# Kernel tuning notes

Measured on AMD Instinct MI355X. Metric: run time of the kernel, lower is better.

The kernel has to match this reference:

```python
import jax, jax.numpy as jnp
import numpy as np

OMODE, PMODE, NZ = 2, 4, 8
NY = NX = 512
NPY = NPX = 128
NPOS = 1024
BATCH = 64


def setup_inputs() -> dict:
    key = jax.random.key(0)
    ks = jax.random.split(key, 8)
    obja = jax.random.uniform(ks[0], (OMODE, NZ, NY, NX), jnp.float32, 0.9, 1.0)
    objp = 0.1 * jax.random.normal(ks[1], (OMODE, NZ, NY, NX), jnp.float32)
    probe = jax.random.normal(ks[2], (PMODE, NPY, NPX, 2), jnp.float32)
    probe_pos_shifts = 0.5 * jax.random.normal(ks[3], (NPOS, 2), jnp.float32)
    theta = jax.random.normal(ks[4], (NPY, NPX), jnp.float32)
    H = jnp.stack([jnp.cos(theta), jnp.sin(theta)], axis=-1)  # unit-modulus Fresnel phasor (re, im)
    omode_occu = jax.nn.softmax(jax.random.normal(ks[5], (OMODE,), jnp.float32))
    indices = jax.random.randint(ks[6], (BATCH,), 0, NPOS, jnp.int32)
    crop_pos = jax.random.randint(ks[7], (NPOS, 2), 0, NY - NPY, jnp.int32)
    return {"obja": obja, "objp": objp, "probe": probe,
            "probe_pos_shifts": probe_pos_shifts, "H": H, "omode_occu": omode_occu,
            "indices": indices, "crop_pos": crop_pos}


def reference(obja, objp, probe, probe_pos_shifts, H, omode_occu, indices, crop_pos):
    npy, npx = probe.shape[1], probe.shape[2]
    probe_c = probe[..., 0] + 1j * probe[..., 1]   # (pmode, Npy, Npx) complex64
    H_c = H[..., 0] + 1j * H[..., 1]               # (Npy, Npx) complex64

    # --- indexed patch gather: (omode, nz, N, Npy, Npx) -> (N, omode, nz, Npy, Npx) ---
    cy = crop_pos[indices, 0]
    cx = crop_pos[indices, 1]
    gy = cy[:, None, None] + jnp.arange(npy, dtype=jnp.int32)[None, :, None]  # (N, Npy, 1)
    gx = cx[:, None, None] + jnp.arange(npx, dtype=jnp.int32)[None, None, :]  # (N, 1, Npx)
    pa = jnp.transpose(obja[:, :, gy, gx], (2, 0, 1, 3, 4))
    pp = jnp.transpose(objp[:, :, gy, gx], (2, 0, 1, 3, 4))
    T = pa * jnp.exp(1j * pp)  # transmission per slice, (N, omode, nz, Npy, Npx)

    # --- sub-pixel Fourier probe shifts (imshift_batch) ---
    kpy = jnp.fft.fftfreq(npy).astype(jnp.float32)
    kpx = jnp.fft.fftfreq(npx).astype(jnp.float32)
    sh = probe_pos_shifts[indices]  # (N, 2)
    ramp = jnp.exp(-2j * jnp.pi * (kpy[None, :, None] * sh[:, 0, None, None]
                                   + kpx[None, None, :] * sh[:, 1, None, None]))  # (N, Npy, Npx)
    probes = jnp.fft.ifft2(jnp.fft.fft2(probe_c)[None] * ramp[:, None])  # (N, pmode, Npy, Npx)

    # --- multislice propagation: psi (N, omode, pmode, Npy, Npx) ---
    psi = probes[:, None]
    nz = T.shape[2]
    for z in range(nz):
        psi = psi * T[:, :, z, None]
        if z < nz - 1:
            psi = jnp.fft.ifft2(jnp.fft.fft2(psi) * H_c)

    # --- far-field detector intensity, mode-incoherent sum ---
    dp = jnp.einsum('o,nopyx->nyx', omode_occu, jnp.abs(jnp.fft.fft2(psi)) ** 2)
    return dp
```

## Files before the change

kernel.cpp:

```cpp
#include <hip/hip_runtime.h>

static constexpr int OMODE = 2, PMODE = 4, NZ = 8;
static constexpr int NYX = 512;
static constexpr int NP  = 128;
static constexpr int BATCH = 64;
static constexpr int LSTR = 129;
static constexpr float INV_N2 = 1.0f / 16384.0f;

typedef float v2f __attribute__((ext_vector_type(2)));

__device__ __forceinline__ int br7(int x) { return (int)(__brev((unsigned)x) >> 25); }

__device__ __forceinline__ v2f splat2(float s) { return (v2f){s, s}; }
__device__ __forceinline__ v2f swapv(v2f v) { return __builtin_shufflevector(v, v, 1, 0); }
__device__ __forceinline__ v2f cmulv(v2f a, float br_, float bi_) {
  return a * splat2(br_) + swapv(a) * (v2f){-bi_, bi_};
}
__device__ __forceinline__ v2f cmulvv(v2f a, v2f b) {
  return a * splat2(b.x) + swapv(a) * (v2f){-b.y, b.y};
}

template<int CTRL>
__device__ __forceinline__ float dppf(float x) {
  int i = __float_as_int(x);
  int r = __builtin_amdgcn_update_dpp(i, i, CTRL, 0xF, 0xF, false);
  return __int_as_float(r);
}

struct Tw {
  float tc6, ts6;
  float g[6];
  float dwr[6], dwi[6];
};

template<int CTRL, int S>
__device__ __forceinline__ v2f bfly_dpp(v2f m, const Tw& tw) {
  v2f t = (v2f){dppf<CTRL>(m.x), dppf<CTRL>(m.y)};
  return t + splat2(tw.g[S]) * m;
}
template<int OFS, int S>
__device__ __forceinline__ v2f bfly_swz(v2f m, const Tw& tw) {
  v2f t;
  t.x = __int_as_float(__builtin_amdgcn_ds_swizzle(__float_as_int(m.x), OFS));
  t.y = __int_as_float(__builtin_amdgcn_ds_swizzle(__float_as_int(m.y), OFS));
  return t + splat2(tw.g[S]) * m;
}
__device__ __forceinline__ v2f bfly_bp32(v2f m, int bp32, float g5) {
  v2f t;
  t.x = __int_as_float(__builtin_amdgcn_ds_bpermute(bp32, __float_as_int(m.x)));
  t.y = __int_as_float(__builtin_amdgcn_ds_bpermute(bp32, __float_as_int(m.y)));
  return t + splat2(g5) * m;
}

template<int S> __device__ __forceinline__ v2f twd(v2f d, const Tw& tw) {
  return d * splat2(tw.dwr[S]) + swapv(d) * (v2f){-tw.dwi[S], tw.dwi[S]};
}
template<int S> __device__ __forceinline__ v2f twc(v2f a, const Tw& tw) {
  return a * splat2(tw.dwr[S]) + swapv(a) * (v2f){tw.dwi[S], -tw.dwi[S]};
}

__device__ __forceinline__ void dif128(v2f& A, v2f& B, const Tw& tw, int bp32) {
  {
    v2f d = A - B;
    A = A + B;
    B = d * splat2(tw.tc6) + swapv(d) * (v2f){tw.ts6, -tw.ts6};
  }
  A = twd<5>(bfly_bp32(A, bp32, tw.g[5]), tw);  B = twd<5>(bfly_bp32(B, bp32, tw.g[5]), tw);
  A = twd<4>(bfly_swz<0x401F, 4>(A, tw), tw);   B = twd<4>(bfly_swz<0x401F, 4>(B, tw), tw);
  A = twd<3>(bfly_swz<0x201F, 3>(A, tw), tw);   B = twd<3>(bfly_swz<0x201F, 3>(B, tw), tw);
  A = twd<2>(bfly_swz<0x101F, 2>(A, tw), tw);   B = twd<2>(bfly_swz<0x101F, 2>(B, tw), tw);
  A = twd<1>(bfly_dpp<0x4E, 1>(A, tw), tw);     B = twd<1>(bfly_dpp<0x4E, 1>(B, tw), tw);
  A = bfly_dpp<0xB1, 0>(A, tw);                 B = bfly_dpp<0xB1, 0>(B, tw);
}

__device__ __forceinline__ void dit128(v2f& A, v2f& B, const Tw& tw, int bp32) {
  A = bfly_dpp<0xB1, 0>(A, tw);                 B = bfly_dpp<0xB1, 0>(B, tw);
  A = bfly_dpp<0x4E, 1>(twc<1>(A, tw), tw);     B = bfly_dpp<0x4E, 1>(twc<1>(B, tw), tw);
  A = bfly_swz<0x101F, 2>(twc<2>(A, tw), tw);   B = bfly_swz<0x101F, 2>(twc<2>(B, tw), tw);
  A = bfly_swz<0x201F, 3>(twc<3>(A, tw), tw);   B = bfly_swz<0x201F, 3>(twc<3>(B, tw), tw);
  A = bfly_swz<0x401F, 4>(twc<4>(A, tw), tw);   B = bfly_swz<0x401F, 4>(twc<4>(B, tw), tw);
  A = bfly_bp32(twc<5>(A, tw), bp32, tw.g[5]);  B = bfly_bp32(twc<5>(B, tw), bp32, tw.g[5]);
  {
    v2f m = B * splat2(tw.tc6) + swapv(B) * (v2f){-tw.ts6, tw.ts6};
    B = A - m;
    A = A + m;
  }
}

__device__ __forceinline__ void init_tw(Tw& tw, int lane) {
  tw.g[0] = (lane & 1) ? -1.f : 1.f;
#pragma unroll
  for (int s = 1; s < 6; ++s) {
    int h = 1 << s;
    int j = lane & (h - 1);
    float ang = 3.14159265358979f * (float)j / (float)h;
    float ts_, tc_;
    __sincosf(ang, &ts_, &tc_);
    bool up = (lane >> s) & 1;
    tw.g[s]   = up ? -1.f : 1.f;
    tw.dwr[s] = up ? tc_ : 1.f;
    tw.dwi[s] = up ? -ts_ : 0.f;
  }
  __sincosf(3.14159265358979f * (float)lane * (1.f / 64.f), &tw.ts6, &tw.tc6);
}

__global__ void __launch_bounds__(256) init_hpre(const float* __restrict__ H,
                                                 float2* __restrict__ hp) {
  int i = blockIdx.x * blockDim.x + threadIdx.x;
  if (i >= NP * NP) return;
  int px = i >> 7, py = i & (NP - 1);
  int ky = br7(py), kx = br7(px);
  hp[px * NP + py] = make_float2(H[(ky * NP + kx) * 2 + 0] * INV_N2,
                                 H[(ky * NP + kx) * 2 + 1] * INV_N2);
}

__global__ void __launch_bounds__(256) init_ramp(const float* __restrict__ shifts,
                                                 const int* __restrict__ indices,
                                                 float2* __restrict__ rampy,
                                                 float2* __restrict__ rampx) {
  int i = blockIdx.x * blockDim.x + threadIdx.x;
  if (i >= 2 * BATCH * NP) return;
  int which = (i >= BATCH * NP) ? 1 : 0;
  int r = i - which * BATCH * NP;
  int n = r >> 7, slot = r & (NP - 1);
  int pos = indices[n];
  float sh = shifts[2 * pos + which];
  int k = br7(slot);
  float f = (float)(k < 64 ? k : k - 128) * (1.f / 128.f);
  float s, c;
  __sincosf(-6.28318530717959f * f * sh, &s, &c);
  if (!which) rampy[n * NP + slot] = make_float2(c * INV_N2, s * INV_N2);
  else        rampx[n * NP + slot] = make_float2(c, s);
}

__global__ void __launch_bounds__(256) init_T(const float* __restrict__ obja,
                                              const float* __restrict__ objp,
                                              float2* __restrict__ T) {
  int i = blockIdx.x * 256 + threadIdx.x;
  if (i >= OMODE * NZ * NYX * NYX) return;
  float a = obja[i], ph = objp[i];
  float s, c;
  __sincosf(ph, &s, &c);
  T[i] = make_float2(a * c, a * s);
}

__global__ void __launch_bounds__(256) reduce_dp(const float* __restrict__ part,
                                                 const float* __restrict__ occu,
                                                 float* __restrict__ dp) {
  int i = blockIdx.x * 256 + threadIdx.x;
  if (i >= BATCH * NP * NP) return;
  int n = i >> 14;
  int r = i & (NP * NP - 1);
  int ky = r >> 7, kx = r & (NP - 1);
  const float* b = part + ((size_t)n * 8 << 14) + (kx << 7) + ky;
  float w0 = occu[0], w1 = occu[1];
  float s = 0.f;
#pragma unroll
  for (int j = 0; j < 8; ++j) s = fmaf(b[(size_t)j << 14], (j < 4 ? w0 : w1), s);
  dp[i] = s;
}

__global__ void
__attribute__((amdgpu_flat_work_group_size(1024, 1024), amdgpu_waves_per_eu(4, 4)))
shift_probe(const float* __restrict__ probe,
            const float2* __restrict__ rampy, const float2* __restrict__ rampx,
            float2* __restrict__ ps)
{
  extern __shared__ v2f fld[];
  const int blk  = blockIdx.x;
  const int n    = blk >> 2;
  const int p    = blk & 3;
  const int tid  = threadIdx.x;
  const int wid  = tid >> 6;
  const int lane = tid & 63;
  const int bp32 = (lane ^ 32) << 2;

  Tw tw;
  init_tw(tw, lane);

  const v2f* probe2 = (const v2f*)probe;
#pragma unroll 1
  for (int k0 = 0; k0 < 8; k0 += 4) {
    int r0 = wid * 8 + k0;
    v2f A[4], B[4];
#pragma unroll
    for (int kk = 0; kk < 4; ++kk) {
      A[kk] = probe2[(p * NP + r0 + kk) * NP + lane];
      B[kk] = probe2[(p * NP + r0 + kk) * NP + lane + 64];
    }
#pragma unroll
    for (int kk = 0; kk < 4; ++kk) dif128(A[kk], B[kk], tw, bp32);
#pragma unroll
    for (int kk = 0; kk < 4; ++kk) {
      fld[(r0 + kk) * LSTR + lane]      = A[kk];
      fld[(r0 + kk) * LSTR + lane + 64] = B[kk];
    }
  }
  __syncthreads();

  {
    float2 t0 = rampy[n * NP + lane];
    float2 t1 = rampy[n * NP + lane + 64];
    v2f ry0 = (v2f){t0.x, t0.y}, ry1 = (v2f){t1.x, t1.y};
#pragma unroll 1
    for (int k0 = 0; k0 < 8; k0 += 4) {
      int c0 = wid * 8 + k0;
      float2 rx[4];
#pragma unroll
      for (int kk = 0; kk < 4; ++kk) rx[kk] = rampx[n * NP + c0 + kk];
      v2f A[4], B[4];
#pragma unroll
      for (int kk = 0; kk < 4; ++kk) {
        A[kk] = fld[lane * LSTR + c0 + kk];
        B[kk] = fld[(lane + 64) * LSTR + c0 + kk];
      }
#pragma unroll
      for (int kk = 0; kk < 4; ++kk) dif128(A[kk], B[kk], tw, bp32);
#pragma unroll
      for (int kk = 0; kk < 4; ++kk) {
        v2f m;
        m = cmulv(ry0, rx[kk].x, rx[kk].y); A[kk] = cmulvv(A[kk], m);
        m = cmulv(ry1, rx[kk].x, rx[kk].y); B[kk] = cmulvv(B[kk], m);
      }
#pragma unroll
      for (int kk = 0; kk < 4; ++kk) dit128(A[kk], B[kk], tw, bp32);
#pragma unroll
      for (int kk = 0; kk < 4; ++kk) {
        fld[lane * LSTR + c0 + kk]        = A[kk];
        fld[(lane + 64) * LSTR + c0 + kk] = B[kk];
      }
    }
    __syncthreads();
  }

  float2* out = ps + ((size_t)blk << 14);
#pragma unroll 1
  for (int k0 = 0; k0 < 8; k0 += 4) {
    int r0 = wid * 8 + k0;
    v2f A[4], B[4];
#pragma unroll
    for (int kk = 0; kk < 4; ++kk) {
      A[kk] = fld[(r0 + kk) * LSTR + lane];
      B[kk] = fld[(r0 + kk) * LSTR + lane + 64];
    }
#pragma unroll
    for (int kk = 0; kk < 4; ++kk) dit128(A[kk], B[kk], tw, bp32);
#pragma unroll
    for (int kk = 0; kk < 4; ++kk) {
      out[(r0 + kk) * NP + lane]      = make_float2(A[kk].x, A[kk].y);
      out[(r0 + kk) * NP + lane + 64] = make_float2(B[kk].x, B[kk].y);
    }
  }
}

__global__ void
__attribute__((amdgpu_flat_work_group_size(1024, 1024), amdgpu_waves_per_eu(4, 4)))
ptycho_chain(
    const float* __restrict__ obja, const float* __restrict__ objp,
    const float* __restrict__ probe, const float* __restrict__ shifts,
    const float* __restrict__ H, const float2* __restrict__ hpre,
    const float2* __restrict__ rampy, const float2* __restrict__ rampx,
    const float2* __restrict__ Tpre, const float2* __restrict__ Ps,
    const float* __restrict__ occu, const int* __restrict__ indices,
    const int* __restrict__ crop, float* __restrict__ dp,
    float* __restrict__ part, int mode_ws, int mode_T, int mode_ps)
{
  extern __shared__ v2f fld[];

  const int blk  = blockIdx.x;
  const int n    = blk >> 3;
  const int o    = (blk >> 2) & 1;
  const int p    = blk & 3;
  const int tid  = threadIdx.x;
  const int wid  = tid >> 6;
  const int lane = tid & 63;
  const int bp32 = (lane ^ 32) << 2;

  const int   pos = indices[n];
  const int   cy  = crop[2 * pos + 0];
  const int   cx  = crop[2 * pos + 1];
  const float wocc = occu[o];

  Tw tw;
  init_tw(tw, lane);

  auto ramp_mul_fb = [&](v2f& A, v2f& B, int c) {
    float sh0v = shifts[2 * pos], sh1v = shifts[2 * pos + 1];
    int kxc = br7(c);
    float fx = (float)(kxc < 64 ? kxc : kxc - 128) * (1.f / 128.f);
    int ky0 = br7(lane);
    float fy0 = (float)(ky0 < 64 ? ky0 : ky0 - 128) * (1.f / 128.f);
    int ky1 = ky0 + 1;
    float fy1 = (float)(ky1 < 64 ? ky1 : ky1 - 128) * (1.f / 128.f);
    float com = fx * sh1v;
    float s0, c0_, s1, c1_;
    __sincosf(-6.28318530717959f * (fy0 * sh0v + com), &s0, &c0_);
    __sincosf(-6.28318530717959f * (fy1 * sh0v + com), &s1, &c1_);
    A = cmulv(A, c0_ * INV_N2, s0 * INV_N2);
    B = cmulv(B, c1_ * INV_N2, s1 * INV_N2);
  };
  auto h_mul_fb = [&](v2f& A, v2f& B, int c) {
    int kx = br7(c), ky0 = br7(lane);
    float hr0 = H[(ky0 * NP + kx) * 2], hi0 = H[(ky0 * NP + kx) * 2 + 1];
    float hr1 = H[((ky0 + 1) * NP + kx) * 2], hi1 = H[((ky0 + 1) * NP + kx) * 2 + 1];
    A = cmulv(A, hr0 * INV_N2, hi0 * INV_N2);
    B = cmulv(B, hr1 * INV_N2, hi1 * INV_N2);
  };

  auto cphase = [&](int mode) {
    v2f ry0, ry1;
    if (mode == 0 && mode_ws) {
      float2 t0 = rampy[n * NP + lane];
      float2 t1 = rampy[n * NP + lane + 64];
      ry0 = (v2f){t0.x, t0.y}; ry1 = (v2f){t1.x, t1.y};
    }
#pragma unroll 1
    for (int k0 = 0; k0 < 8; k0 += 4) {
      int c0 = wid * 8 + k0;
      float2 h0[4], h1[4], rx[4];
      if (mode == 1 && mode_ws) {
#pragma unroll
        for (int kk = 0; kk < 4; ++kk) {
          h0[kk] = hpre[(c0 + kk) * NP + lane];
          h1[kk] = hpre[(c0 + kk) * NP + lane + 64];
        }
      }
      if (mode == 0 && mode_ws) {
#pragma unroll
        for (int kk = 0; kk < 4; ++kk) rx[kk] = rampx[n * NP + c0 + kk];
      }
      v2f A[4], B[4];
#pragma unroll
      for (int kk = 0; kk < 4; ++kk) {
        A[kk] = fld[lane * LSTR + c0 + kk];
        B[kk] = fld[(lane + 64) * LSTR + c0 + kk];
      }
#pragma unroll
      for (int kk = 0; kk < 4; ++kk) dif128(A[kk], B[kk], tw, bp32);
      if (mode == 0) {
        if (mode_ws) {
#pragma unroll
          for (int kk = 0; kk < 4; ++kk) {
            v2f m;
            m = cmulv(ry0, rx[kk].x, rx[kk].y); A[kk] = cmulvv(A[kk], m);
            m = cmulv(ry1, rx[kk].x, rx[kk].y); B[kk] = cmulvv(B[kk], m);
          }
        } else {
#pragma unroll
          for (int kk = 0; kk < 4; ++kk) ramp_mul_fb(A[kk], B[kk], c0 + kk);
        }
      } else {
        if (mode_ws) {
#pragma unroll
          for (int kk = 0; kk < 4; ++kk) {
            A[kk] = cmulv(A[kk], h0[kk].x, h0[kk].y);
            B[kk] = cmulv(B[kk], h1[kk].x, h1[kk].y);
          }
        } else {
#pragma unroll
          for (int kk = 0; kk < 4; ++kk) h_mul_fb(A[kk], B[kk], c0 + kk);
        }
      }
#pragma unroll
      for (int kk = 0; kk < 4; ++kk) dit128(A[kk], B[kk], tw, bp32);
#pragma unroll
      for (int kk = 0; kk < 4; ++kk) {
        fld[lane * LSTR + c0 + kk]        = A[kk];
        fld[(lane + 64) * LSTR + c0 + kk] = B[kk];
      }
    }
    __syncthreads();
  };

  auto rphase = [&](int z) {
#pragma unroll 1
    for (int k0 = 0; k0 < 8; k0 += 4) {
      int r0 = wid * 8 + k0;
      size_t ob = ((size_t)(o * NZ + z) * NYX + (size_t)(cy + r0)) * NYX + cx;
      v2f A[4], B[4];
#pragma unroll
      for (int kk = 0; kk < 4; ++kk) {
        A[kk] = fld[(r0 + kk) * LSTR + lane];
        B[kk] = fld[(r0 + kk) * LSTR + lane + 64];
      }
      if (mode_T) {
        float2 t0[4], t1[4];
#pragma unroll
        for (int kk = 0; kk < 4; ++kk) {
          t0[kk] = Tpre[ob + (size_t)kk * NYX + lane];
          t1[kk] = Tpre[ob + (size_t)kk * NYX + lane + 64];
        }
        dit128(A[0], B[0], tw, bp32); dit128(A[1], B[1], tw, bp32);
        dit128(A[2], B[2], tw, bp32); dit128(A[3], B[3], tw, bp32);
#pragma unroll
        for (int kk = 0; kk < 4; ++kk) {
          A[kk] = cmulv(A[kk], t0[kk].x, t0[kk].y);
          B[kk] = cmulv(B[kk], t1[kk].x, t1[kk].y);
        }
      } else {
        float pa0[4], ph0[4], pa1[4], ph1[4];
#pragma unroll
        for (int kk = 0; kk < 4; ++kk) {
          pa0[kk] = obja[ob + (size_t)kk * NYX + lane];
          ph0[kk] = objp[ob + (size_t)kk * NYX + lane];
          pa1[kk] = obja[ob + (size_t)kk * NYX + lane + 64];
          ph1[kk] = objp[ob + (size_t)kk * NYX + lane + 64];
        }
        dit128(A[0], B[0], tw, bp32); dit128(A[1], B[1], tw, bp32);
        dit128(A[2], B[2], tw, bp32); dit128(A[3], B[3], tw, bp32);
#pragma unroll
        for (int kk = 0; kk < 4; ++kk) {
          float s, c;
          __sincosf(ph0[kk], &s, &c); A[kk] = cmulv(A[kk], pa0[kk] * c, pa0[kk] * s);
          __sincosf(ph1[kk], &s, &c); B[kk] = cmulv(B[kk], pa1[kk] * c, pa1[kk] * s);
        }
      }
#pragma unroll
      for (int kk = 0; kk < 4; ++kk) dif128(A[kk], B[kk], tw, bp32);
#pragma unroll
      for (int kk = 0; kk < 4; ++kk) {
        fld[(r0 + kk) * LSTR + lane]      = A[kk];
        fld[(r0 + kk) * LSTR + lane + 64] = B[kk];
      }
    }
    __syncthreads();
  };

  if (mode_ps) {
    const float2* psf = Ps + ((size_t)((n << 2) + p) << 14);
#pragma unroll 1
    for (int k0 = 0; k0 < 8; k0 += 4) {
      int r0 = wid * 8 + k0;
      size_t ob = ((size_t)(o * NZ + 0) * NYX + (size_t)(cy + r0)) * NYX + cx;
      v2f A[4], B[4];
#pragma unroll
      for (int kk = 0; kk < 4; ++kk) {
        float2 p0 = psf[(r0 + kk) * NP + lane];
        float2 p1 = psf[(r0 + kk) * NP + lane + 64];
        float2 t0 = Tpre[ob + (size_t)kk * NYX + lane];
        float2 t1 = Tpre[ob + (size_t)kk * NYX + lane + 64];
        A[kk] = cmulv((v2f){p0.x, p0.y}, t0.x, t0.y);
        B[kk] = cmulv((v2f){p1.x, p1.y}, t1.x, t1.y);
      }
#pragma unroll
      for (int kk = 0; kk < 4; ++kk) dif128(A[kk], B[kk], tw, bp32);
#pragma unroll
      for (int kk = 0; kk < 4; ++kk) {
        fld[(r0 + kk) * LSTR + lane]      = A[kk];
        fld[(r0 + kk) * LSTR + lane + 64] = B[kk];
      }
    }
    __syncthreads();
  } else {
    const v2f* probe2 = (const v2f*)probe;
#pragma unroll 1
    for (int k0 = 0; k0 < 8; k0 += 4) {
      int r0 = wid * 8 + k0;
      v2f A[4], B[4];
#pragma unroll
      for (int kk = 0; kk < 4; ++kk) {
        A[kk] = probe2[(p * NP + r0 + kk) * NP + lane];
        B[kk] = probe2[(p * NP + r0 + kk) * NP + lane + 64];
      }
#pragma unroll
      for (int kk = 0; kk < 4; ++kk) dif128(A[kk], B[kk], tw, bp32);
#pragma unroll
      for (int kk = 0; kk < 4; ++kk) {
        fld[(r0 + kk) * LSTR + lane]      = A[kk];
        fld[(r0 + kk) * LSTR + lane + 64] = B[kk];
      }
    }
    __syncthreads();
    cphase(0);
    rphase(0);
  }

#pragma unroll 1
  for (int z = 1; z < NZ; ++z) {
    cphase(1);
    rphase(z);
  }

#pragma unroll 1
  for (int k0 = 0; k0 < 8; k0 += 4) {
    int c0 = wid * 8 + k0;
    v2f A[4], B[4];
#pragma unroll
    for (int kk = 0; kk < 4; ++kk) {
      A[kk] = fld[lane * LSTR + c0 + kk];
      B[kk] = fld[(lane + 64) * LSTR + c0 + kk];
    }
#pragma unroll
    for (int kk = 0; kk < 4; ++kk) dif128(A[kk], B[kk], tw, bp32);
    int ky0 = br7(lane);
#pragma unroll
    for (int kk = 0; kk < 4; ++kk) {
      float m0 = fmaf(A[kk].x, A[kk].x, A[kk].y * A[kk].y);
      float m1 = fmaf(B[kk].x, B[kk].x, B[kk].y * B[kk].y);
      if (mode_ws) {
        size_t b0 = ((size_t)blk << 14) + (size_t)br7(c0 + kk) * NP;
        part[b0 + ky0]     = m0;
        part[b0 + ky0 + 1] = m1;
      } else {
        size_t base = ((size_t)n << 14);
        atomicAdd(&dp[base + (size_t)ky0 * NP + br7(c0 + kk)],       m0 * wocc);
        atomicAdd(&dp[base + (size_t)(ky0 + 1) * NP + br7(c0 + kk)], m1 * wocc);
      }
    }
  }
}

extern "C" void kernel_launch(void* const* d_in, const int* in_sizes, int n_in,
                              void* d_out, int out_size, void* d_ws, size_t ws_size,
                              hipStream_t stream) {
  const float* obja   = (const float*)d_in[0];
  const float* objp   = (const float*)d_in[1];
  const float* probe  = (const float*)d_in[2];
  const float* shifts = (const float*)d_in[3];
  const float* H      = (const float*)d_in[4];
  const float* occu   = (const float*)d_in[5];
  const int*   indices = (const int*)d_in[6];
  const int*   crop    = (const int*)d_in[7];
  float* dp = (float*)d_out;

  const size_t part_bytes  = (size_t)BATCH * OMODE * PMODE * NP * NP * sizeof(float);
  const size_t hpre_bytes  = (size_t)NP * NP * sizeof(float2);
  const size_t ramp_bytes  = (size_t)BATCH * NP * sizeof(float2);
  const size_t T_bytes     = (size_t)OMODE * NZ * NYX * NYX * sizeof(float2);
  const size_t ps_bytes    = (size_t)BATCH * PMODE * NP * NP * sizeof(float2);
  const size_t need_ws = part_bytes + hpre_bytes + 2 * ramp_bytes;
  const size_t need_T  = need_ws + T_bytes;
  const size_t need_ps = need_T + ps_bytes;

  int mode_ws = (ws_size >= need_ws) ? 1 : 0;
  int mode_T  = (ws_size >= need_T) ? 1 : 0;
  int mode_ps = (ws_size >= need_ps) ? 1 : 0;
  float*  part  = (float*)d_ws;
  float2* hpre  = (float2*)((char*)d_ws + part_bytes);
  float2* rampy = (float2*)((char*)d_ws + part_bytes + hpre_bytes);
  float2* rampx = (float2*)((char*)d_ws + part_bytes + hpre_bytes + ramp_bytes);
  float2* Tpre  = (float2*)((char*)d_ws + need_ws);
  float2* Ps    = (float2*)((char*)d_ws + need_T);

  if (mode_ws) {
    hipLaunchKernelGGL(init_hpre, dim3((NP * NP + 255) / 256), dim3(256), 0,
                       stream, H, hpre);
    hipLaunchKernelGGL(init_ramp, dim3((2 * BATCH * NP + 255) / 256), dim3(256), 0,
                       stream, shifts, indices, rampy, rampx);
  } else {
    hipMemsetAsync(d_out, 0, (size_t)out_size * sizeof(float), stream);
  }
  if (mode_T) {
    hipLaunchKernelGGL(init_T, dim3((OMODE * NZ * NYX * NYX + 255) / 256), dim3(256),
                       0, stream, obja, objp, Tpre);
  }

  const int lds_bytes = NP * LSTR * (int)sizeof(float2);
  if (mode_ps) {
    hipFuncSetAttribute((const void*)shift_probe,
                        hipFuncAttributeMaxDynamicSharedMemorySize, lds_bytes);
    hipLaunchKernelGGL(shift_probe, dim3(BATCH * PMODE), dim3(1024),
                       lds_bytes, stream, probe, rampy, rampx, Ps);
  }

  hipFuncSetAttribute((const void*)ptycho_chain,
                      hipFuncAttributeMaxDynamicSharedMemorySize, lds_bytes);
  hipLaunchKernelGGL(ptycho_chain, dim3(BATCH * OMODE * PMODE), dim3(1024),
                     lds_bytes, stream,
                     obja, objp, probe, shifts, H, hpre, rampy, rampx, Tpre, Ps,
                     occu, indices, crop, dp, part, mode_ws, mode_T, mode_ps);
  if (mode_ws) {
    hipLaunchKernelGGL(reduce_dp, dim3((BATCH * NP * NP + 255) / 256), dim3(256),
                       0, stream, part, occu, dp);
  }
}
```

Measured before the change: 383.8 us.

## Batch eight FFT rows per wave and halve block size to 512 threads

Each wave now processes 8 row/column pairs per iteration instead of 4, and the butterfly stages are restructured to issue all cross-lane swizzle/bpermute/DPP ops for the 8 rows before the dependent arithmetic. The intent is to hide cross-lane permute latency through more independent work per wave. To keep the same coverage, workgroups shrink from 1024 to 512 threads with waves_per_eu lowered from 4 to 2. That trades occupancy for instruction-level parallelism and raises register pressure, with some risk of spills.

```diff
diff --git a/kernel.cpp b/kernel.cpp
--- a/kernel.cpp
+++ b/kernel.cpp
@@ -26,6 +26,23 @@
   int r = __builtin_amdgcn_update_dpp(i, i, CTRL, 0xF, 0xF, false);
   return __int_as_float(r);
 }
+template<int CTRL>
+__device__ __forceinline__ v2f dpp2(v2f v) {
+  return (v2f){dppf<CTRL>(v.x), dppf<CTRL>(v.y)};
+}
+template<int OFS>
+__device__ __forceinline__ v2f swz2(v2f v) {
+  v2f t;
+  t.x = __int_as_float(__builtin_amdgcn_ds_swizzle(__float_as_int(v.x), OFS));
+  t.y = __int_as_float(__builtin_amdgcn_ds_swizzle(__float_as_int(v.y), OFS));
+  return t;
+}
+__device__ __forceinline__ v2f bp2(v2f v, int bp32) {
+  v2f t;
+  t.x = __int_as_float(__builtin_amdgcn_ds_bpermute(bp32, __float_as_int(v.x)));
+  t.y = __int_as_float(__builtin_amdgcn_ds_bpermute(bp32, __float_as_int(v.y)));
+  return t;
+}
 
 struct Tw {
   float tc6, ts6;
@@ -33,25 +50,6 @@
   float dwr[6], dwi[6];
 };
 
-template<int CTRL, int S>
-__device__ __forceinline__ v2f bfly_dpp(v2f m, const Tw& tw) {
-  v2f t = (v2f){dppf<CTRL>(m.x), dppf<CTRL>(m.y)};
-  return t + splat2(tw.g[S]) * m;
-}
-template<int OFS, int S>
-__device__ __forceinline__ v2f bfly_swz(v2f m, const Tw& tw) {
-  v2f t;
-  t.x = __int_as_float(__builtin_amdgcn_ds_swizzle(__float_as_int(m.x), OFS));
-  t.y = __int_as_float(__builtin_amdgcn_ds_swizzle(__float_as_int(m.y), OFS));
-  return t + splat2(tw.g[S]) * m;
-}
-__device__ __forceinline__ v2f bfly_bp32(v2f m, int bp32, float g5) {
-  v2f t;
-  t.x = __int_as_float(__builtin_amdgcn_ds_bpermute(bp32, __float_as_int(m.x)));
-  t.y = __int_as_float(__builtin_amdgcn_ds_bpermute(bp32, __float_as_int(m.y)));
-  return t + splat2(g5) * m;
-}
-
 template<int S> __device__ __forceinline__ v2f twd(v2f d, const Tw& tw) {
   return d * splat2(tw.dwr[S]) + swapv(d) * (v2f){-tw.dwi[S], tw.dwi[S]};
 }
@@ -59,31 +57,94 @@
   return a * splat2(tw.dwr[S]) + swapv(a) * (v2f){tw.dwi[S], -tw.dwi[S]};
 }
 
-__device__ __forceinline__ void dif128(v2f& A, v2f& B, const Tw& tw, int bp32) {
+#define DIF_SWZ_STAGE8(OFS, S)                                             \
+  {                                                                        \
+    v2f tA[8], tB[8];                                                      \
+    _Pragma("unroll") for (int k = 0; k < 8; ++k) {                        \
+      tA[k] = swz2<OFS>(A[k]);                                            \
+      tB[k] = swz2<OFS>(B[k]);                                            \
+    }                                                                      \
+    _Pragma("unroll") for (int k = 0; k < 8; ++k) {                        \
+      A[k] = twd<S>(tA[k] + splat2(tw.g[S]) * A[k], tw);                   \
+      B[k] = twd<S>(tB[k] + splat2(tw.g[S]) * B[k], tw);                   \
+    }                                                                      \
+  }
+
+#define DIT_SWZ_STAGE8(OFS, S)                                             \
+  {                                                                        \
+    v2f mA[8], mB[8], tA[8], tB[8];                                        \
+    _Pragma("unroll") for (int k = 0; k < 8; ++k) {                        \
+      mA[k] = twc<S>(A[k], tw);                                           \
+      mB[k] = twc<S>(B[k], tw);                                           \
+    }                                                                      \
+    _Pragma("unroll") for (int k = 0; k < 8; ++k) {                        \
+      tA[k] = swz2<OFS>(mA[k]);                                           \
+      tB[k] = swz2<OFS>(mB[k]);                                           \
+    }                                                                      \
+    _Pragma("unroll") for (int k = 0; k < 8; ++k) {                        \
+      A[k] = tA[k] + splat2(tw.g[S]) * mA[k];                              \
+      B[k] = tB[k] + splat2(tw.g[S]) * mB[k];                              \
+    }                                                                      \
+  }
+
+__device__ __forceinline__ void dif128_x8(v2f A[8], v2f B[8], const Tw& tw, int bp32) {
+#pragma unroll
+  for (int k = 0; k < 8; ++k) {
+    v2f d = A[k] - B[k];
+    A[k] = A[k] + B[k];
+    B[k] = d * splat2(tw.tc6) + swapv(d) * (v2f){tw.ts6, -tw.ts6};
+  }
   {
-    v2f d = A - B;
-    A = A + B;
-    B = d * splat2(tw.tc6) + swapv(d) * (v2f){tw.ts6, -tw.ts6};
-  }
-  A = twd<5>(bfly_bp32(A, bp32, tw.g[5]), tw);  B = twd<5>(bfly_bp32(B, bp32, tw.g[5]), tw);
-  A = twd<4>(bfly_swz<0x401F, 4>(A, tw), tw);   B = twd<4>(bfly_swz<0x401F, 4>(B, tw), tw);
-  A = twd<3>(bfly_swz<0x201F, 3>(A, tw), tw);   B = twd<3>(bfly_swz<0x201F, 3>(B, tw), tw);
-  A = twd<2>(bfly_swz<0x101F, 2>(A, tw), tw);   B = twd<2>(bfly_swz<0x101F, 2>(B, tw), tw);
-  A = twd<1>(bfly_dpp<0x4E, 1>(A, tw), tw);     B = twd<1>(bfly_dpp<0x4E, 1>(B, tw), tw);
-  A = bfly_dpp<0xB1, 0>(A, tw);                 B = bfly_dpp<0xB1, 0>(B, tw);
-}
-
-__device__ __forceinline__ void dit128(v2f& A, v2f& B, const Tw& tw, int bp32) {
-  A = bfly_dpp<0xB1, 0>(A, tw);                 B = bfly_dpp<0xB1, 0>(B, tw);
-  A = bfly_dpp<0x4E, 1>(twc<1>(A, tw), tw);     B = bfly_dpp<0x4E, 1>(twc<1>(B, tw), tw);
-  A = bfly_swz<0x101F, 2>(twc<2>(A, tw), tw);   B = bfly_swz<0x101F, 2>(twc<2>(B, tw), tw);
-  A = bfly_swz<0x201F, 3>(twc<3>(A, tw), tw);   B = bfly_swz<0x201F, 3>(twc<3>(B, tw), tw);
-  A = bfly_swz<0x401F, 4>(twc<4>(A, tw), tw);   B = bfly_swz<0x401F, 4>(twc<4>(B, tw), tw);
-  A = bfly_bp32(twc<5>(A, tw), bp32, tw.g[5]);  B = bfly_bp32(twc<5>(B, tw), bp32, tw.g[5]);
+    v2f tA[8], tB[8];
+#pragma unroll
+    for (int k = 0; k < 8; ++k) { tA[k] = bp2(A[k], bp32); tB[k] = bp2(B[k], bp32); }
+#pragma unroll
+    for (int k = 0; k < 8; ++k) {
+      A[k] = twd<5>(tA[k] + splat2(tw.g[5]) * A[k], tw);
+      B[k] = twd<5>(tB[k] + splat2(tw.g[5]) * B[k], tw);
+    }
+  }
+  DIF_SWZ_STAGE8(0x401F, 4)
+  DIF_SWZ_STAGE8(0x201F, 3)
+  DIF_SWZ_STAGE8(0x101F, 2)
+#pragma unroll
+  for (int k = 0; k < 8; ++k) {
+    A[k] = twd<1>(dpp2<0x4E>(A[k]) + splat2(tw.g[1]) * A[k], tw);
+    B[k] = twd<1>(dpp2<0x4E>(B[k]) + splat2(tw.g[1]) * B[k], tw);
+    A[k] = dpp2<0xB1>(A[k]) + splat2(tw.g[0]) * A[k];
+    B[k] = dpp2<0xB1>(B[k]) + splat2(tw.g[0]) * B[k];
+  }
+}
+
+__device__ __forceinline__ void dit128_x8(v2f A[8], v2f B[8], const Tw& tw, int bp32) {
+#pragma unroll
+  for (int k = 0; k < 8; ++k) {
+    A[k] = dpp2<0xB1>(A[k]) + splat2(tw.g[0]) * A[k];
+    B[k] = dpp2<0xB1>(B[k]) + splat2(tw.g[0]) * B[k];
+    v2f mA = twc<1>(A[k], tw), mB = twc<1>(B[k], tw);
+    A[k] = dpp2<0x4E>(mA) + splat2(tw.g[1]) * mA;
+    B[k] = dpp2<0x4E>(mB) + splat2(tw.g[1]) * mB;
+  }
+  DIT_SWZ_STAGE8(0x101F, 2)
+  DIT_SWZ_STAGE8(0x201F, 3)
+  DIT_SWZ_STAGE8(0x401F, 4)
   {
-    v2f m = B * splat2(tw.tc6) + swapv(B) * (v2f){-tw.ts6, tw.ts6};
-    B = A - m;
-    A = A + m;
+    v2f mA[8], mB[8], tA[8], tB[8];
+#pragma unroll
+    for (int k = 0; k < 8; ++k) { mA[k] = twc<5>(A[k], tw); mB[k] = twc<5>(B[k], tw); }
+#pragma unroll
+    for (int k = 0; k < 8; ++k) { tA[k] = bp2(mA[k], bp32); tB[k] = bp2(mB[k], bp32); }
+#pragma unroll
+    for (int k = 0; k < 8; ++k) {
+      A[k] = tA[k] + splat2(tw.g[5]) * mA[k];
+      B[k] = tB[k] + splat2(tw.g[5]) * mB[k];
+    }
+  }
+#pragma unroll
+  for (int k = 0; k < 8; ++k) {
+    v2f m = B[k] * splat2(tw.tc6) + swapv(B[k]) * (v2f){-tw.ts6, tw.ts6};
+    B[k] = A[k] - m;
+    A[k] = A[k] + m;
   }
 }
 
@@ -161,7 +222,7 @@
 }
 
 __global__ void
-__attribute__((amdgpu_flat_work_group_size(1024, 1024), amdgpu_waves_per_eu(4, 4)))
+__attribute__((amdgpu_flat_work_group_size(512, 512), amdgpu_waves_per_eu(2, 2)))
 shift_probe(const float* __restrict__ probe,
             const float2* __restrict__ rampy, const float2* __restrict__ rampx,
             float2* __restrict__ ps)
@@ -180,18 +241,17 @@
 
   const v2f* probe2 = (const v2f*)probe;
 #pragma unroll 1
-  for (int k0 = 0; k0 < 8; k0 += 4) {
-    int r0 = wid * 8 + k0;
-    v2f A[4], B[4];
-#pragma unroll
-    for (int kk = 0; kk < 4; ++kk) {
+  for (int k0 = 0; k0 < 16; k0 += 8) {
+    int r0 = wid * 16 + k0;
+    v2f A[8], B[8];
+#pragma unroll
+    for (int kk = 0; kk < 8; ++kk) {
       A[kk] = probe2[(p * NP + r0 + kk) * NP + lane];
       B[kk] = probe2[(p * NP + r0 + kk) * NP + lane + 64];
     }
-#pragma unroll
-    for (int kk = 0; kk < 4; ++kk) dif128(A[kk], B[kk], tw, bp32);
-#pragma unroll
-    for (int kk = 0; kk < 4; ++kk) {
+    dif128_x8(A, B, tw, bp32);
+#pragma unroll
+    for (int kk = 0; kk < 8; ++kk) {
       fld[(r0 + kk) * LSTR + lane]      = A[kk];
       fld[(r0 + kk) * LSTR + lane + 64] = B[kk];
     }
@@ -203,29 +263,27 @@
     float2 t1 = rampy[n * NP + lane + 64];
     v2f ry0 = (v2f){t0.x, t0.y}, ry1 = (v2f){t1.x, t1.y};
 #pragma unroll 1
-    for (int k0 = 0; k0 < 8; k0 += 4) {
-      int c0 = wid * 8 + k0;
-      float2 rx[4];
-#pragma unroll
-      for (int kk = 0; kk < 4; ++kk) rx[kk] = rampx[n * NP + c0 + kk];
-      v2f A[4], B[4];
-#pragma unroll
-      for (int kk = 0; kk < 4; ++kk) {
+    for (int k0 = 0; k0 < 16; k0 += 8) {
+      int c0 = wid * 16 + k0;
+      float2 rx[8];
+#pragma unroll
+      for (int kk = 0; kk < 8; ++kk) rx[kk] = rampx[n * NP + c0 + kk];
+      v2f A[8], B[8];
+#pragma unroll
+      for (int kk = 0; kk < 8; ++kk) {
         A[kk] = fld[lane * LSTR + c0 + kk];
         B[kk] = fld[(lane + 64) * LSTR + c0 + kk];
       }
-#pragma unroll
-      for (int kk = 0; kk < 4; ++kk) dif128(A[kk], B[kk], tw, bp32);
-#pragma unroll
-      for (int kk = 0; kk < 4; ++kk) {
+      dif128_x8(A, B, tw, bp32);
+#pragma unroll
+      for (int kk = 0; kk < 8; ++kk) {
         v2f m;
         m = cmulv(ry0, rx[kk].x, rx[kk].y); A[kk] = cmulvv(A[kk], m);
         m = cmulv(ry1, rx[kk].x, rx[kk].y); B[kk] = cmulvv(B[kk], m);
       }
-#pragma unroll
-      for (int kk = 0; kk < 4; ++kk) dit128(A[kk], B[kk], tw, bp32);
-#pragma unroll
-      for (int kk = 0; kk < 4; ++kk) {
+      dit128_x8(A, B, tw, bp32);
+#pragma unroll
+      for (int kk = 0; kk < 8; ++kk) {
         fld[lane * LSTR + c0 + kk]        = A[kk];
         fld[(lane + 64) * LSTR + c0 + kk] = B[kk];
       }
@@ -235,18 +293,17 @@
 
   float2* out = ps + ((size_t)blk << 14);
 #pragma unroll 1
-  for (int k0 = 0; k0 < 8; k0 += 4) {
-    int r0 = wid * 8 + k0;
-    v2f A[4], B[4];
-#pragma unroll
-    for (int kk = 0; kk < 4; ++kk) {
+  for (int k0 = 0; k0 < 16; k0 += 8) {
+    int r0 = wid * 16 + k0;
+    v2f A[8], B[8];
+#pragma unroll
+    for (int kk = 0; kk < 8; ++kk) {
       A[kk] = fld[(r0 + kk) * LSTR + lane];
       B[kk] = fld[(r0 + kk) * LSTR + lane + 64];
     }
-#pragma unroll
-    for (int kk = 0; kk < 4; ++kk) dit128(A[kk], B[kk], tw, bp32);
-#pragma unroll
-    for (int kk = 0; kk < 4; ++kk) {
+    dit128_x8(A, B, tw, bp32);
+#pragma unroll
+    for (int kk = 0; kk < 8; ++kk) {
       out[(r0 + kk) * NP + lane]      = make_float2(A[kk].x, A[kk].y);
       out[(r0 + kk) * NP + lane + 64] = make_float2(B[kk].x, B[kk].y);
     }
@@ -254,7 +311,7 @@
 }
 
 __global__ void
-__attribute__((amdgpu_flat_work_group_size(1024, 1024), amdgpu_waves_per_eu(4, 4)))
+__attribute__((amdgpu_flat_work_group_size(512, 512), amdgpu_waves_per_eu(2, 2)))
 ptycho_chain(
     const float* __restrict__ obja, const float* __restrict__ objp,
     const float* __restrict__ probe, const float* __restrict__ shifts,
@@ -315,56 +372,54 @@
       ry0 = (v2f){t0.x, t0.y}; ry1 = (v2f){t1.x, t1.y};
     }
 #pragma unroll 1
-    for (int k0 = 0; k0 < 8; k0 += 4) {
-      int c0 = wid * 8 + k0;
-      float2 h0[4], h1[4], rx[4];
+    for (int k0 = 0; k0 < 16; k0 += 8) {
+      int c0 = wid * 16 + k0;
+      float2 h0[8], h1[8], rx[8];
       if (mode == 1 && mode_ws) {
 #pragma unroll
-        for (int kk = 0; kk < 4; ++kk) {
+        for (int kk = 0; kk < 8; ++kk) {
           h0[kk] = hpre[(c0 + kk) * NP + lane];
           h1[kk] = hpre[(c0 + kk) * NP + lane + 64];
         }
       }
       if (mode == 0 && mode_ws) {
 #pragma unroll
-        for (int kk = 0; kk < 4; ++kk) rx[kk] = rampx[n * NP + c0 + kk];
-      }
-      v2f A[4], B[4];
-#pragma unroll
-      for (int kk = 0; kk < 4; ++kk) {
+        for (int kk = 0; kk < 8; ++kk) rx[kk] = rampx[n * NP + c0 + kk];
+      }
+      v2f A[8], B[8];
+#pragma unroll
+      for (int kk = 0; kk < 8; ++kk) {
         A[kk] = fld[lane * LSTR + c0 + kk];
         B[kk] = fld[(lane + 64) * LSTR + c0 + kk];
       }
-#pragma unroll
-      for (int kk = 0; kk < 4; ++kk) dif128(A[kk], B[kk], tw, bp32);
+      dif128_x8(A, B, tw, bp32);
       if (mode == 0) {
         if (mode_ws) {
 #pragma unroll
-          for (int kk = 0; kk < 4; ++kk) {
+          for (int kk = 0; kk < 8; ++kk) {
             v2f m;
             m = cmulv(ry0, rx[kk].x, rx[kk].y); A[kk] = cmulvv(A[kk], m);
             m = cmulv(ry1, rx[kk].x, rx[kk].y); B[kk] = cmulvv(B[kk], m);
           }
         } else {
 #pragma unroll
-          for (int kk = 0; kk < 4; ++kk) ramp_mul_fb(A[kk], B[kk], c0 + kk);
+          for (int kk = 0; kk < 8; ++kk) ramp_mul_fb(A[kk], B[kk], c0 + kk);
         }
       } else {
         if (mode_ws) {
 #pragma unroll
-          for (int kk = 0; kk < 4; ++kk) {
+          for (int kk = 0; kk < 8; ++kk) {
             A[kk] = cmulv(A[kk], h0[kk].x, h0[kk].y);
             B[kk] = cmulv(B[kk], h1[kk].x, h1[kk].y);
           }
         } else {
 #pragma unroll
-          for (int kk = 0; kk < 4; ++kk) h_mul_fb(A[kk], B[kk], c0 + kk);
+          for (int kk = 0; kk < 8; ++kk) h_mul_fb(A[kk], B[kk], c0 + kk);
         }
       }
-#pragma unroll
-      for (int kk = 0; kk < 4; ++kk) dit128(A[kk], B[kk], tw, bp32);
-#pragma unroll
-      for (int kk = 0; kk < 4; ++kk) {
+      dit128_x8(A, B, tw, bp32);
+#pragma unroll
+      for (int kk = 0; kk < 8; ++kk) {
         fld[lane * LSTR + c0 + kk]        = A[kk];
         fld[(lane + 64) * LSTR + c0 + kk] = B[kk];
       }
@@ -374,51 +429,48 @@
 
   auto rphase = [&](int z) {
 #pragma unroll 1
-    for (int k0 = 0; k0 < 8; k0 += 4) {
-      int r0 = wid * 8 + k0;
+    for (int k0 = 0; k0 < 16; k0 += 8) {
+      int r0 = wid * 16 + k0;
       size_t ob = ((size_t)(o * NZ + z) * NYX + (size_t)(cy + r0)) * NYX + cx;
-      v2f A[4], B[4];
-#pragma unroll
-      for (int kk = 0; kk < 4; ++kk) {
+      v2f A[8], B[8];
+#pragma unroll
+      for (int kk = 0; kk < 8; ++kk) {
         A[kk] = fld[(r0 + kk) * LSTR + lane];
         B[kk] = fld[(r0 + kk) * LSTR + lane + 64];
       }
       if (mode_T) {
-        float2 t0[4], t1[4];
-#pragma unroll
-        for (int kk = 0; kk < 4; ++kk) {
+        float2 t0[8], t1[8];
+#pragma unroll
+        for (int kk = 0; kk < 8; ++kk) {
           t0[kk] = Tpre[ob + (size_t)kk * NYX + lane];
           t1[kk] = Tpre[ob + (size_t)kk * NYX + lane + 64];
         }
-        dit128(A[0], B[0], tw, bp32); dit128(A[1], B[1], tw, bp32);
-        dit128(A[2], B[2], tw, bp32); dit128(A[3], B[3], tw, bp32);
-#pragma unroll
-        for (int kk = 0; kk < 4; ++kk) {
+        dit128_x8(A, B, tw, bp32);
+#pragma unroll
+        for (int kk = 0; kk < 8; ++kk) {
           A[kk] = cmulv(A[kk], t0[kk].x, t0[kk].y);
           B[kk] = cmulv(B[kk], t1[kk].x, t1[kk].y);
         }
       } else {
-        float pa0[4], ph0[4], pa1[4], ph1[4];
-#pragma unroll
-        for (int kk = 0; kk < 4; ++kk) {
+        float pa0[8], ph0[8], pa1[8], ph1[8];
+#pragma unroll
+        for (int kk = 0; kk < 8; ++kk) {
           pa0[kk] = obja[ob + (size_t)kk * NYX + lane];
           ph0[kk] = objp[ob + (size_t)kk * NYX + lane];
           pa1[kk] = obja[ob + (size_t)kk * NYX + lane + 64];
           ph1[kk] = objp[ob + (size_t)kk * NYX + lane + 64];
         }
-        dit128(A[0], B[0], tw, bp32); dit128(A[1], B[1], tw, bp32);
-        dit128(A[2], B[2], tw, bp32); dit128(A[3], B[3], tw, bp32);
-#pragma unroll
-        for (int kk = 0; kk < 4; ++kk) {
+        dit128_x8(A, B, tw, bp32);
+#pragma unroll
+        for (int kk = 0; kk < 8; ++kk) {
           float s, c;
           __sincosf(ph0[kk], &s, &c); A[kk] = cmulv(A[kk], pa0[kk] * c, pa0[kk] * s);
           __sincosf(ph1[kk], &s, &c); B[kk] = cmulv(B[kk], pa1[kk] * c, pa1[kk] * s);
         }
       }
-#pragma unroll
-      for (int kk = 0; kk < 4; ++kk) dif128(A[kk], B[kk], tw, bp32);
-#pragma unroll
-      for (int kk = 0; kk < 4; ++kk) {
+      dif128_x8(A, B, tw, bp32);
+#pragma unroll
+      for (int kk = 0; kk < 8; ++kk) {
         fld[(r0 + kk) * LSTR + lane]      = A[kk];
         fld[(r0 + kk) * LSTR + lane + 64] = B[kk];
       }
@@ -429,12 +481,12 @@
   if (mode_ps) {
     const float2* psf = Ps + ((size_t)((n << 2) + p) << 14);
 #pragma unroll 1
-    for (int k0 = 0; k0 < 8; k0 += 4) {
-      int r0 = wid * 8 + k0;
+    for (int k0 = 0; k0 < 16; k0 += 8) {
+      int r0 = wid * 16 + k0;
       size_t ob = ((size_t)(o * NZ + 0) * NYX + (size_t)(cy + r0)) * NYX + cx;
-      v2f A[4], B[4];
-#pragma unroll
-      for (int kk = 0; kk < 4; ++kk) {
+      v2f A[8], B[8];
+#pragma unroll
+      for (int kk = 0; kk < 8; ++kk) {
         float2 p0 = psf[(r0 + kk) * NP + lane];
         float2 p1 = psf[(r0 + kk) * NP + lane + 64];
         float2 t0 = Tpre[ob + (size_t)kk * NYX + lane];
@@ -442,10 +494,9 @@
         A[kk] = cmulv((v2f){p0.x, p0.y}, t0.x, t0.y);
         B[kk] = cmulv((v2f){p1.x, p1.y}, t1.x, t1.y);
       }
-#pragma unroll
-      for (int kk = 0; kk < 4; ++kk) dif128(A[kk], B[kk], tw, bp32);
-#pragma unroll
-      for (int kk = 0; kk < 4; ++kk) {
+      dif128_x8(A, B, tw, bp32);
+#pragma unroll
+      for (int kk = 0; kk < 8; ++kk) {
         fld[(r0 + kk) * LSTR + lane]      = A[kk];
         fld[(r0 + kk) * LSTR + lane + 64] = B[kk];
       }
@@ -454,18 +505,17 @@
   } else {
     const v2f* probe2 = (const v2f*)probe;
 #pragma unroll 1
-    for (int k0 = 0; k0 < 8; k0 += 4) {
-      int r0 = wid * 8 + k0;
-      v2f A[4], B[4];
-#pragma unroll
-      for (int kk = 0; kk < 4; ++kk) {
+    for (int k0 = 0; k0 < 16; k0 += 8) {
+      int r0 = wid * 16 + k0;
+      v2f A[8], B[8];
+#pragma unroll
+      for (int kk = 0; kk < 8; ++kk) {
         A[kk] = probe2[(p * NP + r0 + kk) * NP + lane];
         B[kk] = probe2[(p * NP + r0 + kk) * NP + lane + 64];
       }
-#pragma unroll
-      for (int kk = 0; kk < 4; ++kk) dif128(A[kk], B[kk], tw, bp32);
-#pragma unroll
-      for (int kk = 0; kk < 4; ++kk) {
+      dif128_x8(A, B, tw, bp32);
+#pragma unroll
+      for (int kk = 0; kk < 8; ++kk) {
         fld[(r0 + kk) * LSTR + lane]      = A[kk];
         fld[(r0 + kk) * LSTR + lane + 64] = B[kk];
       }
@@ -482,19 +532,18 @@
   }
 
 #pragma unroll 1
-  for (int k0 = 0; k0 < 8; k0 += 4) {
-    int c0 = wid * 8 + k0;
-    v2f A[4], B[4];
-#pragma unroll
-    for (int kk = 0; kk < 4; ++kk) {
+  for (int k0 = 0; k0 < 16; k0 += 8) {
+    int c0 = wid * 16 + k0;
+    v2f A[8], B[8];
+#pragma unroll
+    for (int kk = 0; kk < 8; ++kk) {
       A[kk] = fld[lane * LSTR + c0 + kk];
       B[kk] = fld[(lane + 64) * LSTR + c0 + kk];
     }
-#pragma unroll
-    for (int kk = 0; kk < 4; ++kk) dif128(A[kk], B[kk], tw, bp32);
+    dif128_x8(A, B, tw, bp32);
     int ky0 = br7(lane);
 #pragma unroll
-    for (int kk = 0; kk < 4; ++kk) {
+    for (int kk = 0; kk < 8; ++kk) {
       float m0 = fmaf(A[kk].x, A[kk].x, A[kk].y * A[kk].y);
       float m1 = fmaf(B[kk].x, B[kk].x, B[kk].y * B[kk].y);
       if (mode_ws) {
@@ -559,13 +608,13 @@
   if (mode_ps) {
     hipFuncSetAttribute((const void*)shift_probe,
                         hipFuncAttributeMaxDynamicSharedMemorySize, lds_bytes);
-    hipLaunchKernelGGL(shift_probe, dim3(BATCH * PMODE), dim3(1024),
+    hipLaunchKernelGGL(shift_probe, dim3(BATCH * PMODE), dim3(512),
                        lds_bytes, stream, probe, rampy, rampx, Ps);
   }
 
   hipFuncSetAttribute((const void*)ptycho_chain,
                       hipFuncAttributeMaxDynamicSharedMemorySize, lds_bytes);
-  hipLaunchKernelGGL(ptycho_chain, dim3(BATCH * OMODE * PMODE), dim3(1024),
+  hipLaunchKernelGGL(ptycho_chain, dim3(BATCH * OMODE * PMODE), dim3(512),
                      lds_bytes, stream,
                      obja, objp, probe, shifts, H, hpre, rampy, rampx, Tpre, Ps,
                      occu, indices, crop, dp, part, mode_ws, mode_T, mode_ps);
```

New measurement: 415.5 us. 8.3% more time.
